# Kernel tuning notes

Measured on AMD Instinct MI355X. Metric: run time of the kernel, lower is better.

Reference implementation:

```python
import jax, jax.numpy as jnp
import numpy as np

N_CLASSES = 64
K_NEIGHBORS = 10
ITERATIONS = 3
IN_DIM = 512
D_MODEL = 256
N_SUPPORT = 2048
N_QUERY = 6144


def setup_inputs() -> dict:
    key = jax.random.key(0)
    k1, k2, k3, k4 = jax.random.split(key, 4)
    support = jax.random.normal(k1, (1, N_SUPPORT, IN_DIM), dtype=jnp.float32)
    query = jax.random.normal(k2, (1, N_QUERY, IN_DIM), dtype=jnp.float32)
    support_labels = jax.random.randint(k3, (N_SUPPORT,), 0, N_CLASSES)
    W = jax.random.normal(k4, (IN_DIM, D_MODEL), dtype=jnp.float32) / np.sqrt(IN_DIM)
    return {"support": support, "query": query, "support_labels": support_labels, "W": W}


def reference(support, query, support_labels, W):
    n_way = N_CLASSES
    ns = support.shape[1]
    nq = query.shape[1]

    # encoder: linear projection
    s_emb = jnp.einsum('bnd,de->bne', support, W)   # (1, ns, D)
    q_emb = jnp.einsum('bnd,de->bne', query, W)     # (1, nq, D)
    all_emb = jnp.concatenate([s_emb, q_emb], axis=1)  # (1, n, D)

    # prototypes (computed in the original forward; unused downstream)
    onehot_s = jax.nn.one_hot(support_labels, n_way, dtype=s_emb.dtype)  # (ns, C)
    counts = onehot_s.sum(0)
    protos = (onehot_s.T @ s_emb[0]) / jnp.maximum(counts, 1.0)[:, None]

    # kNN graph via cdist + topk(smallest) + scatter
    x = all_emb[0]                                  # (n, D)
    n = x.shape[0]
    sq = jnp.sum(x * x, axis=-1)
    d2 = sq[:, None] + sq[None, :] - 2.0 * (x @ x.T)
    dist = jnp.sqrt(jnp.maximum(d2, 0.0))           # (n, n)
    k = min(K_NEIGHBORS, n - 1)
    _, idx = jax.lax.top_k(-dist, k)                # k nearest (incl. self)
    adj = jnp.zeros((n, n), dtype=jnp.float32)
    adj = adj.at[jnp.arange(n)[:, None], idx].set(1.0)
    adj = ((adj + adj.T) > 0).astype(jnp.float32)   # symmetrize

    # row-normalized transition and label propagation
    deg = adj.sum(axis=1, keepdims=True)
    deg = jnp.where(deg == 0, 1.0, deg)
    trans = adj / deg
    label_mat = jnp.concatenate(
        [onehot_s, jnp.zeros((nq, n_way), dtype=jnp.float32)], axis=0)  # (n, C)
    labels = label_mat
    for _ in range(ITERATIONS):
        labels = trans @ labels

    pred = jnp.argmax(labels, axis=-1)              # (n,)
    query_pred = pred[ns:]
    logits = jax.nn.one_hot(query_pred, n_way, dtype=jnp.float32)[None]  # (1, nq, C)
    # protos participates in the original forward; keep it live (no-op add of zeros)
    logits = logits + 0.0 * jnp.sum(protos) * 0.0
    return logits
```

## Files before the change

kernel.cpp:

```cpp
#include <hip/hip_runtime.h>
#include <stdint.h>

#define NS   2048
#define NQ   6144
#define NN   8192
#define IND  512
#define DM   256
#define KNB  10
#define NSPLIT 8
#define PCAP 1536

#define AS1 __attribute__((address_space(1)))
#define AS3 __attribute__((address_space(3)))

typedef short bf16x8 __attribute__((ext_vector_type(8)));
typedef float f32x4  __attribute__((ext_vector_type(4)));
typedef unsigned long long u64;

__device__ __forceinline__ unsigned short f2bf(float v)
{
    unsigned int u = __float_as_uint(v);
    unsigned int r = (u + 0x7fffu + ((u >> 16) & 1u)) >> 16;
    return (unsigned short)r;
}
__device__ __forceinline__ float bf2f(unsigned short h)
{
    return __uint_as_float(((unsigned int)h) << 16);
}

__device__ __forceinline__ void topk_insert(float v, int j, float bval[KNB], int bidx[KNB])
{
    bool better = (v < bval[KNB-1]) || (v == bval[KNB-1] && j < bidx[KNB-1]);
    if (better) {
        float cv = v; int ci = j;
#pragma unroll
        for (int q = 0; q < KNB; ++q) {
            bool sw = (cv < bval[q]) || (cv == bval[q] && ci < bidx[q]);
            if (sw) {
                float tv = bval[q]; bval[q] = cv; cv = tv;
                int   ti = bidx[q]; bidx[q] = ci; ci = ti;
            }
        }
    }
}

__device__ __forceinline__ void key_insert(u64 key, u64 K[KNB])
{
    u64 cur = key;
#pragma unroll
    for (int s = 0; s < KNB; ++s) {
        u64 lo = (cur < K[s]) ? cur : K[s];
        u64 hi = (cur < K[s]) ? K[s] : cur;
        K[s] = lo; cur = hi;
    }
}

__global__ __launch_bounds__(256) void embed_kernel(
    const float* __restrict__ support, const float* __restrict__ query,
    const float* __restrict__ W, bf16x8* __restrict__ Ghi, bf16x8* __restrict__ Glo,
    float* __restrict__ sqpart)
{
    __shared__ float smem[64 * 68];
    __shared__ float sqred[64 * 17];
    float* smemA = smem;
    float* smemB = smem + 32 * 68;
    const int t  = threadIdx.x;
    const int i0 = blockIdx.x * 64;
    const int n0 = blockIdx.y * 64;
    const int tx = t & 15, ty = t >> 4;

    float acc[4][4];
#pragma unroll
    for (int m = 0; m < 4; ++m)
#pragma unroll
        for (int n = 0; n < 4; ++n) acc[m][n] = 0.f;

    for (int kc = 0; kc < IND; kc += 32) {
        {
            int a  = t >> 2;
            int cg = (t & 3) * 8;
            int g  = i0 + a;
            const float* src = (g < NS) ? (support + (size_t)g * IND)
                                        : (query + (size_t)(g - NS) * IND);
            src += kc + cg;
#pragma unroll
            for (int q = 0; q < 2; ++q) {
                float4 v = *reinterpret_cast<const float4*>(src + q * 4);
                smemA[(cg + q*4 + 0) * 68 + a] = v.x;
                smemA[(cg + q*4 + 1) * 68 + a] = v.y;
                smemA[(cg + q*4 + 2) * 68 + a] = v.z;
                smemA[(cg + q*4 + 3) * 68 + a] = v.w;
            }
        }
        {
            int r  = t >> 3;
            int cg = (t & 7) * 8;
            const float* src = W + (size_t)(kc + r) * DM + n0 + cg;
#pragma unroll
            for (int q = 0; q < 2; ++q) {
                float4 v = *reinterpret_cast<const float4*>(src + q * 4);
                *reinterpret_cast<float4*>(&smemB[r * 68 + cg + q * 4]) = v;
            }
        }
        __syncthreads();
#pragma unroll
        for (int kk = 0; kk < 32; ++kk) {
            float4 a0 = *reinterpret_cast<const float4*>(&smemA[kk * 68 + ty * 4]);
            float4 b0 = *reinterpret_cast<const float4*>(&smemB[kk * 68 + tx * 4]);
            float af[4] = {a0.x, a0.y, a0.z, a0.w};
            float bf[4] = {b0.x, b0.y, b0.z, b0.w};
#pragma unroll
            for (int m = 0; m < 4; ++m)
#pragma unroll
                for (int n = 0; n < 4; ++n)
                    acc[m][n] += af[m] * bf[n];
        }
        __syncthreads();
    }
#pragma unroll
    for (int m = 0; m < 4; ++m) {
        float s = 0.f;
#pragma unroll
        for (int n = 0; n < 4; ++n) {
            float v = acc[m][n];
            s += v * v;
            smem[(ty * 4 + m) * 68 + tx * 4 + n] = v;
        }
        sqred[(ty * 4 + m) * 17 + tx] = s;
    }
    __syncthreads();
#pragma unroll
    for (int e = 0; e < 2; ++e) {
        int g  = t * 2 + e;
        int rl = g >> 3;
        int ch = (g >> 2) & 1;
        int qq = g & 3;
        const float* ep = &smem[rl * 68 + ch * 32 + qq * 8];
        bf16x8 h8, l8;
#pragma unroll
        for (int jj = 0; jj < 8; ++jj) {
            float v = ep[jj];
            unsigned short hu = f2bf(v);
            float hf = bf2f(hu);
            unsigned short lu = f2bf(v - hf);
            h8[jj] = (short)hu;
            l8[jj] = (short)lu;
        }
        int cc = blockIdx.y * 2 + ch;
        size_t gi = ((size_t)(cc * 4 + qq)) * NN + (i0 + rl);
        Ghi[gi] = h8;
        Glo[gi] = l8;
    }
    if (t < 64) {
        float s = 0.f;
#pragma unroll
        for (int x = 0; x < 16; ++x) s += sqred[t * 17 + x];
        sqpart[(size_t)blockIdx.y * NN + i0 + t] = s;
    }
}

__global__ __launch_bounds__(256) void sqsum_kernel(const float* __restrict__ sqpart,
                                                    float* __restrict__ sq)
{
    int i = blockIdx.x * 256 + threadIdx.x;
    sq[i] = ((sqpart[i] + sqpart[NN + i]) + sqpart[2 * NN + i]) + sqpart[3 * NN + i];
}

__global__ __launch_bounds__(256, 2) void dist_topk_kernel(
    const bf16x8* __restrict__ Ghi, const bf16x8* __restrict__ Glo,
    const float* __restrict__ sq, float* __restrict__ cval, int* __restrict__ cidx)
{
    __shared__ bf16x8 stage[2][1024];
    __shared__ u64 stk[4][256];
    const int t  = threadIdx.x;
    const int l  = t & 63, w = t >> 6;
    const int lm = l & 15, q = l >> 4;
    const int i0 = blockIdx.x * 64;
    const int row = i0 + 16 * w + lm;
    const int split = blockIdx.y;

    const float  sqi    = sq[row];
    const size_t rowIdx = (size_t)q * NN + row;

    u64 K[KNB];
#pragma unroll
    for (int s = 0; s < KNB; ++s) K[s] = ~0ull;
    u64 thr = ~0ull;
    int cnt = 0;

    auto drain = [&]() {
        u64 live = __ballot(cnt > 0);
        while (live) {
            if (cnt > 0) {
                --cnt;
                u64 key = stk[cnt][t];
                if (key < thr) {
                    key_insert(key, K);
                    thr = K[KNB - 1];
                }
            }
            live = __ballot(cnt > 0);
        }
    };

    auto stage_issue = [&](int it, int b) {
        const int jt = split * 8 + (it >> 3);
        const int c  = it & 7;
        const int j0 = jt * 128;
        const size_t cbase = (size_t)c * (NN * 4);
        const bool hi = (w < 2);
        const int  wf = (w & 1) * 256;
        const bf16x8* gsel = hi ? Ghi : Glo;
#pragma unroll
        for (int u = 0; u < 4; ++u) {
            const int f  = wf + u * 64;
            const int qr = f >> 7, col0 = f & 127;
            const bf16x8* g = gsel + cbase + (size_t)qr * NN + j0 + col0 + l;
            __builtin_amdgcn_global_load_lds((const AS1 void*)g,
                                             (AS3 void*)&stage[b][(hi ? 0 : 512) + f],
                                             16, 0, 0);
        }
    };

    stage_issue(0, 0);
    __syncthreads();

    f32x4 acc[8];
    for (int it = 0; it < 64; ++it) {
        const int c = it & 7;
        const int b = it & 1;
        if (it + 1 < 64) stage_issue(it + 1, (it + 1) & 1);
        if (c == 0) {
#pragma unroll
            for (int mt = 0; mt < 8; ++mt) acc[mt] = (f32x4){0.f, 0.f, 0.f, 0.f};
        }
        const size_t co = (size_t)c * (NN * 4);
        const bf16x8 Bh = Ghi[co + rowIdx];
        const bf16x8 Bl = Glo[co + rowIdx];
        const bf16x8* sh = &stage[b][0];
        const bf16x8* sl = &stage[b][512];
        const int fq = q * 128 + lm;
#pragma unroll
        for (int mt = 0; mt < 8; ++mt) {
            const int fi = fq + 16 * mt;
            const bf16x8 Ah = sh[fi];
            const bf16x8 Al = sl[fi];
            f32x4 a = acc[mt];
            a = __builtin_amdgcn_mfma_f32_16x16x32_bf16(Ah, Bh, a, 0, 0, 0);
            a = __builtin_amdgcn_mfma_f32_16x16x32_bf16(Ah, Bl, a, 0, 0, 0);
            a = __builtin_amdgcn_mfma_f32_16x16x32_bf16(Al, Bh, a, 0, 0, 0);
            a = __builtin_amdgcn_mfma_f32_16x16x32_bf16(Al, Bl, a, 0, 0, 0);
            acc[mt] = a;
        }
        if (c == 7) {
            const int j0 = split * 1024 + (it >> 3) * 128;
#pragma unroll
            for (int mt = 0; mt < 8; ++mt) {
                const int jb = j0 + 16 * mt + 4 * q;
                const f32x4 sqj = *reinterpret_cast<const f32x4*>(&sq[jb]);
#pragma unroll
                for (int r = 0; r < 4; ++r) {
                    float d2 = fmaxf(sqi + sqj[r] - 2.0f * acc[mt][r], 0.0f);
                    u64 key = ((u64)__float_as_uint(d2) << 32) | (unsigned)(jb + r);
                    if (key < thr) { stk[cnt][t] = key; ++cnt; }
                }
                drain();
            }
        }
        __syncthreads();
    }
    u64* dump = reinterpret_cast<u64*>(&stage[0][0]);
#pragma unroll
    for (int s = 0; s < KNB; ++s) dump[t * KNB + s] = K[s];
    if (q == 0) {
#pragma unroll
        for (int qq = 1; qq < 4; ++qq)
#pragma unroll
            for (int s = 0; s < KNB; ++s) {
                u64 key = dump[(t + qq * 16) * KNB + s];
                if (key < thr) {
                    key_insert(key, K);
                    thr = K[KNB - 1];
                }
            }
        size_t base = (size_t)row * (NSPLIT * KNB) + split * KNB;
#pragma unroll
        for (int s = 0; s < KNB; ++s) {
            cval[base + s] = __uint_as_float((unsigned)(K[s] >> 32));
            cidx[base + s] = (int)(K[s] & 0xFFFFFFFFu);
        }
    }
}

__global__ __launch_bounds__(256) void merge_adj_kernel(
    const float* __restrict__ cval, const int* __restrict__ cidx,
    unsigned int* __restrict__ bits)
{
    int i = blockIdx.x * blockDim.x + threadIdx.x;
    if (i >= NN) return;
    float bval[KNB]; int bidx[KNB];
#pragma unroll
    for (int s = 0; s < KNB; ++s) { bval[s] = 3.0e38f; bidx[s] = 0x7fffffff; }
    for (int s = 0; s < NSPLIT * KNB; ++s) {
        float v = cval[(size_t)i * (NSPLIT * KNB) + s];
        int   j = cidx[(size_t)i * (NSPLIT * KNB) + s];
        topk_insert(v, j, bval, bidx);
    }
#pragma unroll
    for (int s = 0; s < KNB; ++s) {
        int j = bidx[s];
        atomicOr(&bits[(size_t)i * 256 + (j >> 5)], 1u << (j & 31));
        atomicOr(&bits[(size_t)j * 256 + (i >> 5)], 1u << (i & 31));
    }
}

__global__ __launch_bounds__(256) void labels_init_kernel(const int* __restrict__ slab, float* __restrict__ la)
{
    int tid = blockIdx.x * blockDim.x + threadIdx.x;
    int i = tid >> 6, c = tid & 63;
    float v = 0.f;
    if (i < NS) v = (slab[i] == c) ? 1.f : 0.f;
    la[tid] = v;
}

__global__ __launch_bounds__(256) void prop_kernel(
    const unsigned int* __restrict__ bits, const float* __restrict__ lin, float* __restrict__ lout)
{
    __shared__ int lists[4][PCAP];
    const int grp = threadIdx.x >> 6;
    const int c   = threadIdx.x & 63;
    const int i   = blockIdx.x * 4 + grp;
    const unsigned int* row = bits + (size_t)i * 256;

    unsigned int mw[4];
#pragma unroll
    for (int k = 0; k < 4; ++k) mw[k] = row[4 * c + k];
    int cnt = __popc(mw[0]) + __popc(mw[1]) + __popc(mw[2]) + __popc(mw[3]);
    int incl = cnt;
#pragma unroll
    for (int d = 1; d < 64; d <<= 1) {
        int nb = __shfl_up(incl, d, 64);
        if (c >= d) incl += nb;
    }
    const int off = incl - cnt;
    const int deg = __shfl(incl, 63, 64);
    const bool use_list = (deg <= PCAP);

    if (use_list) {
        int p = off;
#pragma unroll
        for (int k = 0; k < 4; ++k) {
            unsigned int m = mw[k];
            while (m) {
                int b = __ffs(m) - 1;
                m &= m - 1;
                lists[grp][p++] = (4 * c + k) * 32 + b;
            }
        }
    }
    __syncthreads();

    const float tinv = 1.0f / (float)deg;
    float acc = 0.f;
    if (use_list) {
        const int* lst = lists[grp];
        int d = 0;
        for (; d + 4 <= deg; d += 4) {
            int j0 = lst[d], j1 = lst[d + 1], j2 = lst[d + 2], j3 = lst[d + 3];
            float x0 = lin[(size_t)j0 * 64 + c];
            float x1 = lin[(size_t)j1 * 64 + c];
            float x2 = lin[(size_t)j2 * 64 + c];
            float x3 = lin[(size_t)j3 * 64 + c];
            acc += __fmul_rn(tinv, x0);
            acc += __fmul_rn(tinv, x1);
            acc += __fmul_rn(tinv, x2);
            acc += __fmul_rn(tinv, x3);
        }
        for (; d < deg; ++d) {
            int j = lst[d];
            acc += __fmul_rn(tinv, lin[(size_t)j * 64 + c]);
        }
    } else {
        for (int w2 = 0; w2 < 256; ++w2) {
            unsigned int m = row[w2];
            while (m) {
                int b = __ffs(m) - 1;
                m &= m - 1;
                int j = w2 * 32 + b;
                acc += __fmul_rn(tinv, lin[(size_t)j * 64 + c]);
            }
        }
    }
    lout[(size_t)i * 64 + c] = acc;
}

__global__ __launch_bounds__(256) void argmax_kernel(const float* __restrict__ labels, float* __restrict__ out)
{
    int q = blockIdx.x * 4 + (threadIdx.x >> 6);
    int c = threadIdx.x & 63;
    float bv = labels[(size_t)(NS + q) * 64 + c];
    int   bi = c;
#pragma unroll
    for (int off = 32; off >= 1; off >>= 1) {
        float ov = __shfl_xor(bv, off, 64);
        int   oi = __shfl_xor(bi, off, 64);
        if (ov > bv || (ov == bv && oi < bi)) { bv = ov; bi = oi; }
    }
    out[(size_t)q * 64 + c] = (c == bi) ? 1.0f : 0.0f;
}

extern "C" void kernel_launch(void* const* d_in, const int* in_sizes, int n_in,
                              void* d_out, int out_size, void* d_ws, size_t ws_size,
                              hipStream_t stream)
{
    const float* support = (const float*)d_in[0];
    const float* query   = (const float*)d_in[1];
    const int*   slab    = (const int*)d_in[2];
    const float* W       = (const float*)d_in[3];
    float* out = (float*)d_out;
    char*  ws  = (char*)d_ws;

    const size_t GHI_OFF = 0;
    const size_t GLO_OFF = 4194304;
    const size_t SQ_OFF  = 8388608;
    const size_t CV_OFF  = 8421376;
    const size_t CI_OFF  = CV_OFF + (size_t)NN * NSPLIT * KNB * 4;

    bf16x8*       Ghi  = (bf16x8*)(ws + GHI_OFF);
    bf16x8*       Glo  = (bf16x8*)(ws + GLO_OFF);
    unsigned int* bits = (unsigned int*)(ws + GHI_OFF);
    float*        sq   = (float*)(ws + SQ_OFF);
    float*        sqp  = (float*)(ws + CV_OFF);
    float*        cval = (float*)(ws + CV_OFF);
    int*          cidx = (int*)  (ws + CI_OFF);
    float*        la   = (float*)(ws + CV_OFF);
    float*        lb   = (float*)(ws + CI_OFF);

    embed_kernel<<<dim3(128, 4), 256, 0, stream>>>(support, query, W, Ghi, Glo, sqp);
    sqsum_kernel<<<NN / 256, 256, 0, stream>>>(sqp, sq);
    dist_topk_kernel<<<dim3(128, NSPLIT), 256, 0, stream>>>(Ghi, Glo, sq, cval, cidx);
    hipMemsetAsync(bits, 0, (size_t)NN * 256 * sizeof(unsigned int), stream);
    merge_adj_kernel<<<NN / 256, 256, 0, stream>>>(cval, cidx, bits);
    labels_init_kernel<<<(NN * 64) / 256, 256, 0, stream>>>(slab, la);
    prop_kernel<<<NN / 4, 256, 0, stream>>>(bits, la, lb);
    prop_kernel<<<NN / 4, 256, 0, stream>>>(bits, lb, la);
    prop_kernel<<<NN / 4, 256, 0, stream>>>(bits, la, lb);
    argmax_kernel<<<NQ / 4, 256, 0, stream>>>(lb, out);
}
```

Baseline: 471.0 us.

## Rewrite embedding projection with split-bf16 MFMA and fuse squared-norm reduction

Replaces the scalar FP32 tiled GEMM that computes the encoder projection with MFMA bf16 instructions, splitting inputs and W into hi/lo bf16 pairs (four MFMAs per tile) to keep near-FP32 accuracy. W is pre-packed by a new small kernel. Each block now covers all 256 output dims for 16 nodes, so the squared norm is reduced in one place and the separate sqsum kernel is removed. An extra barrier is added in dist_topk before reusing stage memory. The risk is more MFMA work from the split products and a 512-block grid with direct global W reads.

```diff
diff --git a/kernel.cpp b/kernel.cpp
--- a/kernel.cpp
+++ b/kernel.cpp
@@ -55,115 +55,125 @@
     }
 }
 
+__global__ __launch_bounds__(256) void wpack_kernel(const float* __restrict__ W,
+                                                    bf16x8* __restrict__ Wthi,
+                                                    bf16x8* __restrict__ Wtlo)
+{
+    int f = blockIdx.x * 256 + threadIdx.x;
+    int dim = f & 255, qp = (f >> 8) & 3, c = f >> 10;
+    int k0 = 32 * c + 8 * qp;
+    bf16x8 h8, l8;
+#pragma unroll
+    for (int j = 0; j < 8; ++j) {
+        float v = W[(size_t)(k0 + j) * DM + dim];
+        unsigned short hu = f2bf(v);
+        float hf = bf2f(hu);
+        unsigned short lu = f2bf(v - hf);
+        h8[j] = (short)hu; l8[j] = (short)lu;
+    }
+    Wthi[f] = h8; Wtlo[f] = l8;
+}
+
 __global__ __launch_bounds__(256) void embed_kernel(
     const float* __restrict__ support, const float* __restrict__ query,
-    const float* __restrict__ W, bf16x8* __restrict__ Ghi, bf16x8* __restrict__ Glo,
-    float* __restrict__ sqpart)
-{
-    __shared__ float smem[64 * 68];
-    __shared__ float sqred[64 * 17];
-    float* smemA = smem;
-    float* smemB = smem + 32 * 68;
-    const int t  = threadIdx.x;
-    const int i0 = blockIdx.x * 64;
-    const int n0 = blockIdx.y * 64;
-    const int tx = t & 15, ty = t >> 4;
-
-    float acc[4][4];
-#pragma unroll
-    for (int m = 0; m < 4; ++m)
-#pragma unroll
-        for (int n = 0; n < 4; ++n) acc[m][n] = 0.f;
-
-    for (int kc = 0; kc < IND; kc += 32) {
-        {
-            int a  = t >> 2;
-            int cg = (t & 3) * 8;
-            int g  = i0 + a;
-            const float* src = (g < NS) ? (support + (size_t)g * IND)
-                                        : (query + (size_t)(g - NS) * IND);
-            src += kc + cg;
-#pragma unroll
-            for (int q = 0; q < 2; ++q) {
-                float4 v = *reinterpret_cast<const float4*>(src + q * 4);
-                smemA[(cg + q*4 + 0) * 68 + a] = v.x;
-                smemA[(cg + q*4 + 1) * 68 + a] = v.y;
-                smemA[(cg + q*4 + 2) * 68 + a] = v.z;
-                smemA[(cg + q*4 + 3) * 68 + a] = v.w;
-            }
-        }
-        {
-            int r  = t >> 3;
-            int cg = (t & 7) * 8;
-            const float* src = W + (size_t)(kc + r) * DM + n0 + cg;
-#pragma unroll
-            for (int q = 0; q < 2; ++q) {
-                float4 v = *reinterpret_cast<const float4*>(src + q * 4);
-                *reinterpret_cast<float4*>(&smemB[r * 68 + cg + q * 4]) = v;
-            }
-        }
-        __syncthreads();
-#pragma unroll
-        for (int kk = 0; kk < 32; ++kk) {
-            float4 a0 = *reinterpret_cast<const float4*>(&smemA[kk * 68 + ty * 4]);
-            float4 b0 = *reinterpret_cast<const float4*>(&smemB[kk * 68 + tx * 4]);
-            float af[4] = {a0.x, a0.y, a0.z, a0.w};
-            float bf[4] = {b0.x, b0.y, b0.z, b0.w};
-#pragma unroll
-            for (int m = 0; m < 4; ++m)
-#pragma unroll
-                for (int n = 0; n < 4; ++n)
-                    acc[m][n] += af[m] * bf[n];
-        }
-        __syncthreads();
-    }
-#pragma unroll
-    for (int m = 0; m < 4; ++m) {
+    const bf16x8* __restrict__ Wthi, const bf16x8* __restrict__ Wtlo,
+    bf16x8* __restrict__ Ghi, bf16x8* __restrict__ Glo, float* __restrict__ sq)
+{
+    __shared__ __align__(16) char lds[36928];
+    bf16x8* Ehf = reinterpret_cast<bf16x8*>(lds);
+    bf16x8* Elf = Ehf + 1024;
+    float*  et  = reinterpret_cast<float*>(lds);
+    float*  sqred = reinterpret_cast<float*>(lds + 32768);
+    const int t = threadIdx.x;
+    const int l = t & 63, w = t >> 6;
+    const int lm = l & 15, q = l >> 4;
+    const int i0 = blockIdx.x * 16;
+
+    {
+        const int node = t & 15;
+        const int g = i0 + node;
+        const float* src = (g < NS) ? (support + (size_t)g * IND)
+                                    : (query + (size_t)(g - NS) * IND);
+#pragma unroll
+        for (int i = 0; i < 4; ++i) {
+            int cq = (t >> 4) + 16 * i;
+            const float* p = src + cq * 8;
+            float4 v0 = *reinterpret_cast<const float4*>(p);
+            float4 v1 = *reinterpret_cast<const float4*>(p + 4);
+            float vv[8] = {v0.x, v0.y, v0.z, v0.w, v1.x, v1.y, v1.z, v1.w};
+            bf16x8 h8, l8;
+#pragma unroll
+            for (int j = 0; j < 8; ++j) {
+                unsigned short hu = f2bf(vv[j]);
+                float hf = bf2f(hu);
+                unsigned short lu = f2bf(vv[j] - hf);
+                h8[j] = (short)hu; l8[j] = (short)lu;
+            }
+            Ehf[cq * 16 + node] = h8;
+            Elf[cq * 16 + node] = l8;
+        }
+    }
+    __syncthreads();
+
+    f32x4 acc[4];
+#pragma unroll
+    for (int nt = 0; nt < 4; ++nt) acc[nt] = (f32x4){0.f, 0.f, 0.f, 0.f};
+    const int dimb = 64 * w + lm;
+    for (int c = 0; c < 16; ++c) {
+        const bf16x8 Anh = Ehf[(c * 4 + q) * 16 + lm];
+        const bf16x8 Anl = Elf[(c * 4 + q) * 16 + lm];
+        const int fb = c * 1024 + q * 256 + dimb;
+#pragma unroll
+        for (int nt = 0; nt < 4; ++nt) {
+            const bf16x8 Wh = Wthi[fb + 16 * nt];
+            const bf16x8 Wl = Wtlo[fb + 16 * nt];
+            f32x4 a = acc[nt];
+            a = __builtin_amdgcn_mfma_f32_16x16x32_bf16(Anh, Wh, a, 0, 0, 0);
+            a = __builtin_amdgcn_mfma_f32_16x16x32_bf16(Anh, Wl, a, 0, 0, 0);
+            a = __builtin_amdgcn_mfma_f32_16x16x32_bf16(Anl, Wh, a, 0, 0, 0);
+            a = __builtin_amdgcn_mfma_f32_16x16x32_bf16(Anl, Wl, a, 0, 0, 0);
+            acc[nt] = a;
+        }
+    }
+    __syncthreads();
+
+#pragma unroll
+    for (int r = 0; r < 4; ++r) {
         float s = 0.f;
 #pragma unroll
-        for (int n = 0; n < 4; ++n) {
-            float v = acc[m][n];
+        for (int nt = 0; nt < 4; ++nt) {
+            float v = acc[nt][r];
+            et[(4 * q + r) * 260 + dimb + 16 * nt] = v;
             s += v * v;
-            smem[(ty * 4 + m) * 68 + tx * 4 + n] = v;
-        }
-        sqred[(ty * 4 + m) * 17 + tx] = s;
-    }
-    __syncthreads();
-#pragma unroll
-    for (int e = 0; e < 2; ++e) {
-        int g  = t * 2 + e;
-        int rl = g >> 3;
-        int ch = (g >> 2) & 1;
-        int qq = g & 3;
-        const float* ep = &smem[rl * 68 + ch * 32 + qq * 8];
+        }
+        sqred[(4 * q + r) * 65 + w * 16 + lm] = s;
+    }
+    __syncthreads();
+
+#pragma unroll
+    for (int i = 0; i < 2; ++i) {
+        int f = t + 256 * i;
+        int node = f & 15, qd = (f >> 4) & 3, cd = f >> 6;
+        const float* ep = &et[node * 260 + 32 * cd + 8 * qd];
         bf16x8 h8, l8;
 #pragma unroll
-        for (int jj = 0; jj < 8; ++jj) {
-            float v = ep[jj];
+        for (int j = 0; j < 8; ++j) {
+            float v = ep[j];
             unsigned short hu = f2bf(v);
             float hf = bf2f(hu);
             unsigned short lu = f2bf(v - hf);
-            h8[jj] = (short)hu;
-            l8[jj] = (short)lu;
-        }
-        int cc = blockIdx.y * 2 + ch;
-        size_t gi = ((size_t)(cc * 4 + qq)) * NN + (i0 + rl);
+            h8[j] = (short)hu; l8[j] = (short)lu;
+        }
+        size_t gi = (size_t)(cd * 4 + qd) * NN + i0 + node;
         Ghi[gi] = h8;
         Glo[gi] = l8;
     }
-    if (t < 64) {
+    if (t < 16) {
         float s = 0.f;
 #pragma unroll
-        for (int x = 0; x < 16; ++x) s += sqred[t * 17 + x];
-        sqpart[(size_t)blockIdx.y * NN + i0 + t] = s;
-    }
-}
-
-__global__ __launch_bounds__(256) void sqsum_kernel(const float* __restrict__ sqpart,
-                                                    float* __restrict__ sq)
-{
-    int i = blockIdx.x * 256 + threadIdx.x;
-    sq[i] = ((sqpart[i] + sqpart[NN + i]) + sqpart[2 * NN + i]) + sqpart[3 * NN + i];
+        for (int x = 0; x < 64; ++x) s += sqred[t * 65 + x];
+        sq[i0 + t] = s;
+    }
 }
 
 __global__ __launch_bounds__(256, 2) void dist_topk_kernel(
@@ -269,6 +279,7 @@
         }
         __syncthreads();
     }
+    __syncthreads();
     u64* dump = reinterpret_cast<u64*>(&stage[0][0]);
 #pragma unroll
     for (int s = 0; s < KNB; ++s) dump[t * KNB + s] = K[s];
@@ -430,14 +441,15 @@
     bf16x8*       Glo  = (bf16x8*)(ws + GLO_OFF);
     unsigned int* bits = (unsigned int*)(ws + GHI_OFF);
     float*        sq   = (float*)(ws + SQ_OFF);
-    float*        sqp  = (float*)(ws + CV_OFF);
+    bf16x8*       Wthi = (bf16x8*)(ws + CV_OFF);
+    bf16x8*       Wtlo = (bf16x8*)(ws + CV_OFF + 262144);
     float*        cval = (float*)(ws + CV_OFF);
     int*          cidx = (int*)  (ws + CI_OFF);
     float*        la   = (float*)(ws + CV_OFF);
     float*        lb   = (float*)(ws + CI_OFF);
 
-    embed_kernel<<<dim3(128, 4), 256, 0, stream>>>(support, query, W, Ghi, Glo, sqp);
-    sqsum_kernel<<<NN / 256, 256, 0, stream>>>(sqp, sq);
+    wpack_kernel<<<64, 256, 0, stream>>>(W, Wthi, Wtlo);
+    embed_kernel<<<512, 256, 0, stream>>>(support, query, Wthi, Wtlo, Ghi, Glo, sq);
     dist_topk_kernel<<<dim3(128, NSPLIT), 256, 0, stream>>>(Ghi, Glo, sq, cval, cidx);
     hipMemsetAsync(bits, 0, (size_t)NN * 256 * sizeof(unsigned int), stream);
     merge_adj_kernel<<<NN / 256, 256, 0, stream>>>(cval, cidx, bits);
```

New measurement: 462.8 us. No clear change (-1.7%).
